# Performance work log

Hardware: AMD Instinct MI355X
Metric: run time of the kernel (lower is better)

## Reference

```python
import jax, jax.numpy as jnp
import numpy as np

B, R, C = 32, 2000, 81
BBOX_STD = np.array([0.1, 0.1, 0.2, 0.2], dtype=np.float32)
SCORE_THRESH = 0.1
IMG_W, IMG_H = 512.0, 384.0


def _decode_boxes(boxes, deltas):
    # boxes: [B,R,4] (x1,y1,x2,y2); deltas: [B,R,C,4] -> decoded [B,R,C,4]
    x1, y1, x2, y2 = boxes[..., 0], boxes[..., 1], boxes[..., 2], boxes[..., 3]
    w = x2 - x1 + 1.0
    h = y2 - y1 + 1.0
    cx = x1 + 0.5 * w
    cy = y1 + 0.5 * h
    dx, dy, dw, dh = deltas[..., 0], deltas[..., 1], deltas[..., 2], deltas[..., 3]
    pcx = dx * w[..., None] + cx[..., None]
    pcy = dy * h[..., None] + cy[..., None]
    pw = jnp.exp(dw) * w[..., None]
    ph = jnp.exp(dh) * h[..., None]
    return jnp.stack(
        [pcx - 0.5 * pw, pcy - 0.5 * ph, pcx + 0.5 * pw - 1.0, pcy + 0.5 * ph - 1.0],
        axis=-1,
    )


def setup_inputs() -> dict:
    key = jax.random.key(0)
    k1, k2, k3 = jax.random.split(key, 3)
    # proposal boxes: random well-formed (x1<=x2, y1<=y2) boxes inside the image
    corners = jax.random.uniform(k1, (B, R, 2, 2), dtype=jnp.float32) * jnp.array(
        [IMG_W, IMG_H], dtype=jnp.float32
    )
    x1y1 = jnp.min(corners, axis=2)
    x2y2 = jnp.max(corners, axis=2)
    rois = jnp.concatenate([jnp.zeros((B, R, 1), jnp.float32), x1y1, x2y2], axis=-1)
    cls_prob = jax.nn.softmax(jax.random.normal(k2, (B, R, C), dtype=jnp.float32) * 2.0, axis=-1)
    bbox_pred = jax.random.normal(k3, (B, R, 4 * C), dtype=jnp.float32) * 0.5
    return {"rois": rois, "cls_prob": cls_prob, "bbox_pred": bbox_pred}


def reference(rois, cls_prob, bbox_pred):
    b, r = rois.shape[0], rois.shape[1]
    c = cls_prob.shape[-1]
    boxes = rois[..., 1:5]  # [B,R,4]
    # delta scaling exactly as original: view(-1,4) * [0.1,0.1,0.2,0.2]
    deltas = (bbox_pred.reshape(-1, 4) * jnp.asarray(BBOX_STD)).reshape(b, r, c, 4)
    pred_boxes = _decode_boxes(boxes, deltas)  # [B,R,C,4]
    pred_boxes = jnp.maximum(pred_boxes, 0.0)  # torch.clamp(FINAL_BBOXES, 0)

    scores = cls_prob[..., 1:]          # skip background class, [B,R,C-1]
    cboxes = pred_boxes[:, :, 1:, :]    # [B,R,C-1,4]

    valid = scores > SCORE_THRESH       # score-threshold filter (inds)
    masked = jnp.where(valid, scores, -jnp.inf)
    order = jnp.argsort(-masked, axis=1)  # per-class descending sort over proposals
    sorted_scores = jnp.take_along_axis(scores, order, axis=1)
    sorted_valid = jnp.take_along_axis(valid, order, axis=1)
    sorted_boxes = jnp.take_along_axis(cboxes, order[..., None], axis=1)

    # cls_dets = [boxes | score], invalid (sub-threshold) rows zeroed instead of dropped
    dets = jnp.concatenate([sorted_boxes, sorted_scores[..., None]], axis=-1)
    dets = dets * sorted_valid[..., None].astype(dets.dtype)  # [B,R,C-1,5]

    # eval branch: softmax over class scores, max + argmax
    distribution = jax.nn.softmax(cls_prob, axis=-1)
    max_scores = jnp.max(distribution, axis=-1)
    pred_labels = jnp.argmax(distribution, axis=-1)
    return dets, sorted_valid, distribution, max_scores, pred_labels
```

## Files before the change

kernel.cpp:

```cpp
#include <hip/hip_runtime.h>
#include <hip/hip_bf16.h>
#include <math.h>

#define BB 32
#define RR 2000
#define CC 81
#define CM1 80
#define TROWS 64
#define NTILE 32
#define NTILES_TOTAL 1024
#define CAP 28
#define SCAP (NTILE * CAP)
#define NCOLS 2560

__global__ __launch_bounds__(256) void fused1_kernel(
    const float* __restrict__ cls,
    const float* __restrict__ rois,
    const float* __restrict__ bbox,
    float* __restrict__ dist,
    float* __restrict__ maxs,
    float* __restrict__ labels,
    float4* __restrict__ zbase,
    int* __restrict__ counts,
    float2* __restrict__ pairs)
{
    __shared__ float tile[CC * (TROWS + 1)];
    const int tid  = threadIdx.x;
    const int wave = tid >> 6;
    const int lane = tid & 63;

    if (blockIdx.x < NTILES_TOTAL) {
        const int b   = blockIdx.x >> 5;
        const int tr  = blockIdx.x & 31;
        const int r0  = tr * TROWS;
        const int nr  = (RR - r0 < TROWS) ? (RR - r0) : TROWS;

        const float* src = cls + (size_t)(b * RR + r0) * CC;
        for (int i = tid; i < nr * CC; i += 256) {
            int rl = i / CC, c = i - rl * CC;
            tile[c * (TROWS + 1) + rl] = src[i];
        }

        if (wave == 0 && lane < nr) {
            const float4 rv = *(const float4*)(rois +
                (size_t)(b * RR + r0 + lane) * 5 + 1);
            asm volatile("" :: "v"(rv.x), "v"(rv.y), "v"(rv.z), "v"(rv.w));
        }
        __syncthreads();

        #pragma unroll 4
        for (int q = 0; q < 20; ++q) {
            const int c   = 1 + wave + 4 * q;
            const int col = b * CM1 + (c - 1);
            float s = tile[c * (TROWS + 1) + lane];
            bool valid = (lane < nr) && (s > 0.1f);
            unsigned long long mask = __ballot(valid);
            if (valid) {
                int pos = __popcll(mask & ((1ull << lane) - 1ull));
                if (pos < CAP)
                    pairs[(size_t)col * SCAP + tr * CAP + pos] =
                        make_float2(s, __int_as_float(r0 + lane));
                const float4 d4 = *(const float4*)(bbox +
                    (size_t)(b * RR + r0 + lane) * (4 * CC) + 4 * c);
                asm volatile("" :: "v"(d4.x), "v"(d4.y), "v"(d4.z), "v"(d4.w));
            }
            if (lane == 0) {
                int cnt = (int)__popcll(mask);
                counts[col * NTILE + tr] = (cnt < CAP) ? cnt : CAP;
            }
        }
        return;
    }

    const int pb = blockIdx.x - NTILES_TOTAL;

    const float4 z4 = make_float4(0.0f, 0.0f, 0.0f, 0.0f);
    const int zb = pb * 480;
    zbase[zb + tid] = z4;
    if (tid < 224) zbase[zb + 256 + tid] = z4;

    const int row = pb * 4 + wave;

    const float* in = cls + (size_t)row * CC;
    float v0 = in[lane];
    float v1 = (lane < CC - 64) ? in[64 + lane] : -INFINITY;

    float m  = v0;
    int   mi = lane;
    if (v1 > m) { m = v1; mi = 64 + lane; }

    for (int off = 32; off > 0; off >>= 1) {
        float om  = __shfl_xor(m, off);
        int   omi = __shfl_xor(mi, off);
        if (om > m || (om == m && omi < mi)) { m = om; mi = omi; }
    }

    float e0 = expf(v0 - m);
    float e1 = (lane < CC - 64) ? expf(v1 - m) : 0.0f;
    float s  = e0 + e1;
    for (int off = 32; off > 0; off >>= 1) s += __shfl_xor(s, off);

    float inv = 1.0f / s;
    float* out = dist + (size_t)row * CC;
    out[lane] = e0 * inv;
    if (lane < CC - 64) out[64 + lane] = e1 * inv;
    if (lane == 0) {
        maxs[row]   = inv;
        labels[row] = (float)mi;
    }
}

__global__ __launch_bounds__(128) void sort_decode_kernel(
    const float* __restrict__ rois,
    const float* __restrict__ bbox,
    const int* __restrict__ counts,
    const float2* __restrict__ pairs,
    float* __restrict__ dets,
    float* __restrict__ sv)
{
    __shared__ float ssc[1024];
    __shared__ int   sidx[1024];
    __shared__ int   scnt[NTILE];
    __shared__ int   spref[NTILE + 1];

    const int bj  = blockIdx.x;
    const int b   = bj / CM1;
    const int j   = bj % CM1;
    const int tid = threadIdx.x;
    const int wave = tid >> 6;
    const int lane = tid & 63;
    const int cls_col = j + 1;

    int c = (lane < NTILE) ? counts[bj * NTILE + lane] : 0;
    int x = c;
    #pragma unroll
    for (int off = 1; off < NTILE; off <<= 1) {
        int v = __shfl_up(x, off);
        if (lane >= off) x += v;
    }
    const int e = x - c;
    const int n = __shfl(x, NTILE - 1);
    if (n == 0) return;

    const float2* pbase = pairs + (size_t)bj * SCAP;

    if (n <= 128) {
        const int g = (wave << 6) | lane;

        int lo = 0;
        #pragma unroll
        for (int st = 16; st > 0; st >>= 1) {
            int p = lo + st;
            int v = __shfl(e, (p < NTILE) ? p : 0);
            if (p < NTILE && v <= g) lo = p;
        }
        int base = __shfl(e, lo);

        float s; int id;
        if (g < n) {
            float2 pr = pbase[lo * CAP + (g - base)];
            s  = pr.x;
            id = __float_as_int(pr.y);
        } else {
            s  = -INFINITY;
            id = 0x7FFFFFFF;
        }

        const bool asc = (wave == 1);
        #pragma unroll
        for (int k = 2; k <= 64; k <<= 1) {
            #pragma unroll
            for (int jj = k >> 1; jj > 0; jj >>= 1) {
                float os = __shfl_xor(s, jj);
                int   oi = __shfl_xor(id, jj);
                bool mineFirst = (s > os) || (s == os && id < oi);
                if (asc) mineFirst = !mineFirst;
                bool iLower = ((lane & jj) == 0);
                bool up = ((lane & k) == 0);
                bool keep = up ? (mineFirst == iLower) : (mineFirst != iLower);
                if (!keep) { s = os; id = oi; }
            }
        }

        ssc[tid]  = s;
        sidx[tid] = id;
        __syncthreads();
        {
            float os = ssc[tid ^ 64];
            int   oi = sidx[tid ^ 64];
            bool mineFirst = (s > os) || (s == os && id < oi);
            bool iLower = (wave == 0);
            if (mineFirst != iLower) { s = os; id = oi; }
        }
        #pragma unroll
        for (int jj = 32; jj > 0; jj >>= 1) {
            float os = __shfl_xor(s, jj);
            int   oi = __shfl_xor(id, jj);
            bool mineFirst = (s > os) || (s == os && id < oi);
            bool iLower = ((lane & jj) == 0);
            if (mineFirst != iLower) { s = os; id = oi; }
        }

        if (g < n) {
            size_t obase = ((size_t)(b * RR + g) * CM1 + j) * 5;
            int   r = id;
            const float* rp = rois + (size_t)(b * RR + r) * 5;
            float x1 = rp[1], y1 = rp[2], x2 = rp[3], y2 = rp[4];
            float w  = x2 - x1 + 1.0f;
            float h  = y2 - y1 + 1.0f;
            float cx = x1 + 0.5f * w;
            float cy = y1 + 0.5f * h;
            const float* dp = bbox + (size_t)(b * RR + r) * (4 * CC) + 4 * cls_col;
            float dx = dp[0] * 0.1f, dy = dp[1] * 0.1f;
            float dw = dp[2] * 0.2f, dh = dp[3] * 0.2f;
            float pcx = dx * w + cx;
            float pcy = dy * h + cy;
            float pw  = expf(dw) * w;
            float ph  = expf(dh) * h;
            dets[obase + 0] = fmaxf(pcx - 0.5f * pw, 0.0f);
            dets[obase + 1] = fmaxf(pcy - 0.5f * ph, 0.0f);
            dets[obase + 2] = fmaxf(pcx + 0.5f * pw - 1.0f, 0.0f);
            dets[obase + 3] = fmaxf(pcy + 0.5f * ph - 1.0f, 0.0f);
            dets[obase + 4] = s;
            sv[(size_t)(b * RR + g) * CM1 + j] = 1.0f;
        }
        return;
    }

    if (wave == 0 && lane < NTILE) {
        scnt[lane]  = c;
        spref[lane] = e;
        if (lane == NTILE - 1) spref[NTILE] = n;
    }
    __syncthreads();

    for (int t = wave; t < NTILE; t += 2) {
        int cnt = scnt[t];
        for (int k = lane; k < cnt; k += 64) {
            float2 pe = pbase[t * CAP + k];
            int pos = spref[t] + k;
            ssc[pos]  = pe.x;
            sidx[pos] = __float_as_int(pe.y);
        }
    }
    __syncthreads();

    int n2 = 1;
    while (n2 < n) n2 <<= 1;
    for (int i = n + tid; i < n2; i += 128) {
        ssc[i]  = -INFINITY;
        sidx[i] = 0x7FFFFFFF;
    }
    __syncthreads();
    for (int k = 2; k <= n2; k <<= 1) {
        for (int jj = k >> 1; jj > 0; jj >>= 1) {
            for (int i = tid; i < n2; i += 128) {
                int ixj = i ^ jj;
                if (ixj > i) {
                    float si = ssc[i], sx = ssc[ixj];
                    int   ii = sidx[i], ix = sidx[ixj];
                    bool before = (si > sx) || (si == sx && ii < ix);
                    bool doswap = ((i & k) == 0) ? !before : before;
                    if (doswap) {
                        ssc[i] = sx; ssc[ixj] = si;
                        sidx[i] = ix; sidx[ixj] = ii;
                    }
                }
            }
            __syncthreads();
        }
    }

    for (int i = tid; i < n; i += 128) {
        size_t obase = ((size_t)(b * RR + i) * CM1 + j) * 5;
        int   r = sidx[i];
        float s = ssc[i];
        const float* rp = rois + (size_t)(b * RR + r) * 5;
        float x1 = rp[1], y1 = rp[2], x2 = rp[3], y2 = rp[4];
        float w  = x2 - x1 + 1.0f;
        float h  = y2 - y1 + 1.0f;
        float cx = x1 + 0.5f * w;
        float cy = y1 + 0.5f * h;
        const float* dp = bbox + (size_t)(b * RR + r) * (4 * CC) + 4 * cls_col;
        float dx = dp[0] * 0.1f, dy = dp[1] * 0.1f;
        float dw = dp[2] * 0.2f, dh = dp[3] * 0.2f;
        float pcx = dx * w + cx;
        float pcy = dy * h + cy;
        float pw  = expf(dw) * w;
        float ph  = expf(dh) * h;
        dets[obase + 0] = fmaxf(pcx - 0.5f * pw, 0.0f);
        dets[obase + 1] = fmaxf(pcy - 0.5f * ph, 0.0f);
        dets[obase + 2] = fmaxf(pcx + 0.5f * pw - 1.0f, 0.0f);
        dets[obase + 3] = fmaxf(pcy + 0.5f * ph - 1.0f, 0.0f);
        dets[obase + 4] = s;
        sv[(size_t)(b * RR + i) * CM1 + j] = 1.0f;
    }
}

extern "C" void kernel_launch(void* const* d_in, const int* in_sizes, int n_in,
                              void* d_out, int out_size, void* d_ws, size_t ws_size,
                              hipStream_t stream) {
    const float* rois = (const float*)d_in[0];
    const float* cls  = (const float*)d_in[1];
    const float* bbox = (const float*)d_in[2];

    float* out = (float*)d_out;
    const size_t sv_off   = (size_t)BB * RR * CM1 * 5;
    const size_t dist_off = sv_off + (size_t)BB * RR * CM1;
    const size_t maxs_off = dist_off + (size_t)BB * RR * CC;
    const size_t lab_off  = maxs_off + (size_t)BB * RR;

    float* dets   = out;
    float* sv     = out + sv_off;
    float* dist   = out + dist_off;
    float* maxs   = out + maxs_off;
    float* labels = out + lab_off;

    int*    counts = (int*)d_ws;
    float2* pairs  = (float2*)((char*)d_ws + (size_t)NCOLS * NTILE * sizeof(int));

    fused1_kernel<<<NTILES_TOTAL + (BB * RR) / 4, 256, 0, stream>>>(
        cls, rois, bbox, dist, maxs, labels, (float4*)dets, counts, pairs);

    sort_decode_kernel<<<NCOLS, 128, 0, stream>>>(
        rois, bbox, counts, pairs, dets, sv);
}
```

Baseline: 45.28 us.

## Split output zero-fill between the first kernel and extra sort-kernel blocks

The zero-fill of the dets and sorted-valid outputs is split in two. The first kernel's softmax blocks zero the front portion of each batch's rows, and new trailing blocks in the sort/decode kernel zero the remaining tail. The aim is to balance memory-write work across both launches and overlap it with the sort work. It adds index division math and many extra blocks. It also depends on the sort kernel only writing to the front region, or writing before the tail zero blocks run; otherwise the order is unclear and results could be wrong.

```diff
diff --git a/kernel.cpp b/kernel.cpp
--- a/kernel.cpp
+++ b/kernel.cpp
@@ -13,6 +13,18 @@
 #define SCAP (NTILE * CAP)
 #define NCOLS 2560
 
+#define DETS_F4_PER_B 200000u
+#define DETS_F4_FRONT  89600u
+#define DETS_F4_TAIL  110400u
+#define SV_F4_BASE   6400000u
+#define SV_F4_PER_B    40000u
+#define SV_F4_FRONT    17920u
+#define SV_F4_TAIL     22080u
+#define FRONT_DETS_TOTAL 2867200u
+#define FRONT_TOTAL      3440640u
+#define TAIL_DETS_TOTAL  3532800u
+#define TAIL_TOTAL       4239360u
+
 __global__ __launch_bounds__(256) void fused1_kernel(
     const float* __restrict__ cls,
     const float* __restrict__ rois,
@@ -20,7 +32,7 @@
     float* __restrict__ dist,
     float* __restrict__ maxs,
     float* __restrict__ labels,
-    float4* __restrict__ zbase,
+    float4* __restrict__ out_f4,
     int* __restrict__ counts,
     float2* __restrict__ pairs)
 {
@@ -74,10 +86,25 @@
 
     const int pb = blockIdx.x - NTILES_TOTAL;
 
-    const float4 z4 = make_float4(0.0f, 0.0f, 0.0f, 0.0f);
-    const int zb = pb * 480;
-    zbase[zb + tid] = z4;
-    if (tid < 224) zbase[zb + 256 + tid] = z4;
+    {
+        const int cnt   = 215 + (pb < 640 ? 1 : 0);
+        const unsigned start = (unsigned)pb * 215u + (unsigned)min(pb, 640);
+        if (tid < cnt) {
+            unsigned fi = start + (unsigned)tid;
+            unsigned addr;
+            if (fi < FRONT_DETS_TOTAL) {
+                unsigned b_  = fi / DETS_F4_FRONT;
+                unsigned off = fi - b_ * DETS_F4_FRONT;
+                addr = b_ * DETS_F4_PER_B + off;
+            } else {
+                unsigned i2  = fi - FRONT_DETS_TOTAL;
+                unsigned b_  = i2 / SV_F4_FRONT;
+                unsigned off = i2 - b_ * SV_F4_FRONT;
+                addr = SV_F4_BASE + b_ * SV_F4_PER_B + off;
+            }
+            out_f4[addr] = make_float4(0.f, 0.f, 0.f, 0.f);
+        }
+    }
 
     const int row = pb * 4 + wave;
 
@@ -110,23 +137,48 @@
     }
 }
 
-__global__ __launch_bounds__(128) void sort_decode_kernel(
+__global__ __launch_bounds__(128) void sort_decode_zero_kernel(
     const float* __restrict__ rois,
     const float* __restrict__ bbox,
     const int* __restrict__ counts,
     const float2* __restrict__ pairs,
     float* __restrict__ dets,
-    float* __restrict__ sv)
+    float* __restrict__ sv,
+    float4* __restrict__ out_f4)
 {
     __shared__ float ssc[1024];
     __shared__ int   sidx[1024];
     __shared__ int   scnt[NTILE];
     __shared__ int   spref[NTILE + 1];
 
+    const int tid = threadIdx.x;
+
+    if (blockIdx.x >= NCOLS) {
+        const unsigned z = blockIdx.x - NCOLS;
+        unsigned base = z * 384u + (unsigned)tid;
+        const float4 z4 = make_float4(0.f, 0.f, 0.f, 0.f);
+        #pragma unroll
+        for (int k = 0; k < 3; ++k) {
+            unsigned ti = base + (unsigned)(k * 128);
+            unsigned addr;
+            if (ti < TAIL_DETS_TOTAL) {
+                unsigned b_  = ti / DETS_F4_TAIL;
+                unsigned off = ti - b_ * DETS_F4_TAIL;
+                addr = b_ * DETS_F4_PER_B + DETS_F4_FRONT + off;
+            } else {
+                unsigned i2  = ti - TAIL_DETS_TOTAL;
+                unsigned b_  = i2 / SV_F4_TAIL;
+                unsigned off = i2 - b_ * SV_F4_TAIL;
+                addr = SV_F4_BASE + b_ * SV_F4_PER_B + SV_F4_FRONT + off;
+            }
+            out_f4[addr] = z4;
+        }
+        return;
+    }
+
     const int bj  = blockIdx.x;
     const int b   = bj / CM1;
     const int j   = bj % CM1;
-    const int tid = threadIdx.x;
     const int wave = tid >> 6;
     const int lane = tid & 63;
     const int cls_col = j + 1;
@@ -320,8 +372,8 @@
     float2* pairs  = (float2*)((char*)d_ws + (size_t)NCOLS * NTILE * sizeof(int));
 
     fused1_kernel<<<NTILES_TOTAL + (BB * RR) / 4, 256, 0, stream>>>(
-        cls, rois, bbox, dist, maxs, labels, (float4*)dets, counts, pairs);
-
-    sort_decode_kernel<<<NCOLS, 128, 0, stream>>>(
-        rois, bbox, counts, pairs, dets, sv);
+        cls, rois, bbox, dist, maxs, labels, (float4*)out, counts, pairs);
+
+    sort_decode_zero_kernel<<<NCOLS + 11040, 128, 0, stream>>>(
+        rois, bbox, counts, pairs, dets, sv, (float4*)out);
 }
```

Result: slower. 50.07 us (+10.6%).
